# Kernel optimization log

Hardware: AMD Instinct MI355X
Metric: run time of the kernel (lower is better)

## Reference

```python
import jax, jax.numpy as jnp
import numpy as np
from jax import lax

D_MODEL = 1024
D_STATE = 16
D_CONV = 4
EXPAND = 2
D_INNER = EXPAND * D_MODEL  # 2048
DT_RANK = -(-D_MODEL // 16)  # ceil = 64
BATCH = 2
T = 1024


def setup_inputs() -> dict:
    key = jax.random.key(0)
    ks = jax.random.split(key, 9)
    s = 0.02
    x = jax.random.normal(ks[0], (BATCH, T, D_MODEL), dtype=jnp.float32)
    W_in = jax.random.normal(ks[1], (D_MODEL, 2 * D_INNER), dtype=jnp.float32) * s
    conv_w = jax.random.normal(ks[2], (D_INNER, D_CONV), dtype=jnp.float32) * 0.2
    conv_b = jax.random.normal(ks[3], (D_INNER,), dtype=jnp.float32) * 0.02
    W_xproj = jax.random.normal(ks[4], (D_INNER, DT_RANK + 2 * D_STATE), dtype=jnp.float32) * s
    W_dt = jax.random.normal(ks[5], (DT_RANK, D_INNER), dtype=jnp.float32) * s
    b_dt = jax.random.normal(ks[6], (D_INNER,), dtype=jnp.float32) * 0.02
    A_log = jnp.broadcast_to(jnp.log(jnp.arange(1, D_STATE + 1, dtype=jnp.float32)), (D_INNER, D_STATE)).copy()
    D_param = jnp.ones((D_INNER,), dtype=jnp.float32)
    W_out = jax.random.normal(ks[7], (D_INNER, D_MODEL), dtype=jnp.float32) * s
    return {"x": x, "W_in": W_in, "conv_w": conv_w, "conv_b": conv_b,
            "W_xproj": W_xproj, "W_dt": W_dt, "b_dt": b_dt,
            "A_log": A_log, "D_param": D_param, "W_out": W_out}


def _silu(u):
    return u * jax.nn.sigmoid(u)


def _forward(x, W_in, conv_w, conv_b, W_xproj, W_dt, b_dt, A_log, D_param, W_out):
    B, Tlen, _ = x.shape
    # in_proj and split into x-branch and gate z
    xz = x @ W_in                                   # (B,T,2*d_inner)
    x_b, z = jnp.split(xz, 2, axis=-1)              # each (B,T,d_inner)
    # causal depthwise conv1d: y[t] = sum_k w[:,k] * x[t-d_conv+1+k]
    xpad = jnp.pad(x_b, ((0, 0), (D_CONV - 1, 0), (0, 0)))
    xc = conv_b
    for k in range(D_CONV):
        xc = xc + xpad[:, k:k + Tlen, :] * conv_w[:, k]
    xc = _silu(xc)                                  # (B,T,d_inner)
    # SSM parameter projections
    proj = xc @ W_xproj                             # (B,T,dt_rank+2*d_state)
    delta_raw = proj[..., :DT_RANK]
    B_in = proj[..., DT_RANK:DT_RANK + D_STATE]     # (B,T,d_state)
    C_in = proj[..., DT_RANK + D_STATE:]            # (B,T,d_state)
    delta = jax.nn.softplus(delta_raw @ W_dt + b_dt)  # (B,T,d_inner)
    A = -jnp.exp(A_log)                             # (d_inner,d_state)
    A_bar = jnp.exp(delta[..., None] * A)           # (B,T,d_inner,d_state)
    Bx = delta[..., None] * B_in[:, :, None, :] * xc[..., None]  # (B,T,d_inner,d_state)

    def step(h, ins):
        a_t, bx_t, c_t, xc_t = ins
        h = a_t * h + bx_t                          # (B,d_inner,d_state)
        y_t = jnp.einsum('bds,bs->bd', h, c_t) + D_param * xc_t
        return h, y_t

    h0 = jnp.zeros((B, D_INNER, D_STATE), dtype=x.dtype)
    ins = (jnp.swapaxes(A_bar, 0, 1), jnp.swapaxes(Bx, 0, 1),
           jnp.swapaxes(C_in, 0, 1), jnp.swapaxes(xc, 0, 1))
    _, ys = lax.scan(step, h0, ins)                 # ys: (T,B,d_inner)
    y = jnp.swapaxes(ys, 0, 1) * _silu(z)           # gated
    return y @ W_out                                # (B,T,d_model)


def reference(x, W_in, conv_w, conv_b, W_xproj, W_dt, b_dt, A_log, D_param, W_out):
    return _forward(x, W_in, conv_w, conv_b, W_xproj, W_dt, b_dt, A_log, D_param, W_out)
```

## Files before the change

kernel.cpp:

```cpp
#include <hip/hip_runtime.h>
#include <math.h>

#define BATCH   2
#define TLEN    1024
#define DMODEL  1024
#define DINNER  2048
#define DSTATE  16
#define DTRANK  64
#define NPROJ   (DTRANK + 2*DSTATE)
#define CH      16
#define NCH     (TLEN / CH)

typedef __attribute__((ext_vector_type(8))) short short8;
typedef __attribute__((ext_vector_type(4))) float f32x4;

__device__ __forceinline__ float siluf(float u) {
    return u / (1.0f + __expf(-u));
}
__device__ __forceinline__ float softplusf(float x) {
    return (x > 20.0f) ? x : log1pf(__expf(x));
}
__device__ __forceinline__ unsigned short f2bf(float f) {
    union { float f; unsigned u; } v; v.f = f;
    unsigned r = v.u + 0x7FFF + ((v.u >> 16) & 1);
    return (unsigned short)(r >> 16);
}
__device__ __forceinline__ float bf2f(unsigned short u) {
    union { unsigned u; float f; } v; v.u = (unsigned)u << 16;
    return v.f;
}

#define GLOAD_LDS16(g, l) \
  __builtin_amdgcn_global_load_lds( \
     (const __attribute__((address_space(1))) unsigned int*)(g), \
     (__attribute__((address_space(3))) unsigned int*)(l), 16, 0, 0)

template<int NFRAG, int OUTBF>
__global__ __launch_bounds__(256)
void gemm_bf16(const unsigned short* __restrict__ A,
               const unsigned short* __restrict__ BT,
               void* __restrict__ Cv, int ldc, int K)
{
    constexpr int BN = NFRAG * 32;
    __shared__ unsigned short As[128 * 32];
    __shared__ unsigned short Bs[BN * 32];

    const int nwg = gridDim.x * gridDim.y;
    int id = blockIdx.y * gridDim.x + blockIdx.x;
    {
        const int q = nwg >> 3, r = nwg & 7, xcd = id & 7, lid = id >> 3;
        id = (xcd < r ? xcd * (q + 1) : r * (q + 1) + (xcd - r) * q) + lid;
    }
    const int bx = id % gridDim.x, by = id / gridDim.x;

    const int tid  = threadIdx.x;
    const int wid  = tid >> 6;
    const int lane = tid & 63;
    const int brow = by * 128;
    const int bcol = bx * BN;
    const int wr = (wid >> 1) * 64;
    const int wc = (wid & 1) * (NFRAG * 16);
    const int lrow = lane & 15;
    const int lk   = (lane >> 4) * 8;

    f32x4 acc[4][NFRAG] = {};

    for (int k0 = 0; k0 < K; k0 += 32) {
        #pragma unroll
        for (int it = 0; it < 2; ++it) {
            const int c = it * 256 + tid;
            const unsigned short* g = A + (size_t)(brow + (c >> 2)) * K + k0 + (c & 3) * 8;
            GLOAD_LDS16(g, As + (size_t)(it * 256 + wid * 64) * 8);
        }
        #pragma unroll
        for (int it = 0; it < BN / 64; ++it) {
            const int c = it * 256 + tid;
            const unsigned short* g = BT + (size_t)(bcol + (c >> 2)) * K + k0 + (c & 3) * 8;
            GLOAD_LDS16(g, Bs + (size_t)(it * 256 + wid * 64) * 8);
        }
        __syncthreads();

        short8 af[4], bfr[NFRAG];
        #pragma unroll
        for (int m = 0; m < 4; ++m)
            af[m] = *(const short8*)(As + (size_t)(wr + m * 16 + lrow) * 32 + lk);
        #pragma unroll
        for (int n = 0; n < NFRAG; ++n)
            bfr[n] = *(const short8*)(Bs + (size_t)(wc + n * 16 + lrow) * 32 + lk);

        #pragma unroll
        for (int m = 0; m < 4; ++m)
            #pragma unroll
            for (int n = 0; n < NFRAG; ++n)
                acc[m][n] = __builtin_amdgcn_mfma_f32_16x16x32_bf16(af[m], bfr[n], acc[m][n], 0, 0, 0);
        __syncthreads();
    }

    const int crow = (lane >> 4) * 4;
    #pragma unroll
    for (int m = 0; m < 4; ++m)
        #pragma unroll
        for (int n = 0; n < NFRAG; ++n) {
            const size_t coff = (size_t)(brow + wr + m * 16 + crow) * ldc + bcol + wc + n * 16 + lrow;
            #pragma unroll
            for (int r = 0; r < 4; ++r) {
                if (OUTBF)
                    ((unsigned short*)Cv)[coff + (size_t)r * ldc] = f2bf(acc[m][n][r]);
                else
                    ((float*)Cv)[coff + (size_t)r * ldc] = acc[m][n][r];
            }
        }
}

template<int EPI, int ABF, int OUTBF>
__global__ __launch_bounds__(256)
void gemm_f32(const void* __restrict__ Av, int lda,
              const float* __restrict__ B, int ldb,
              void* __restrict__ Cv, int ldc,
              int N, int kchunk,
              const float* __restrict__ bias, size_t zstride)
{
    __shared__ float As[16][64 + 4];
    __shared__ float Bs[16][64 + 4];
    const int tid  = threadIdx.x;
    const int brow = blockIdx.y * 64;
    const int bcol = blockIdx.x * 64;
    const int kbeg = blockIdx.z * kchunk;
    const size_t cofs = (size_t)blockIdx.z * zstride;
    const int tr = ((tid >> 4) & 15) << 2;
    const int tc = (tid & 15) << 2;
    const int ar = tid >> 2;
    const int ac = (tid & 3) << 2;
    const int br = tid >> 4;
    const int bc = (tid & 15) << 2;

    float acc[4][4] = {{0.f,0.f,0.f,0.f},{0.f,0.f,0.f,0.f},
                       {0.f,0.f,0.f,0.f},{0.f,0.f,0.f,0.f}};

    for (int k0 = kbeg; k0 < kbeg + kchunk; k0 += 16) {
        float4 av;
        if (ABF) {
            const unsigned short* Ab = (const unsigned short*)Av;
            ushort4 t = *(const ushort4*)(Ab + (size_t)(brow + ar) * lda + k0 + ac);
            av = make_float4(bf2f(t.x), bf2f(t.y), bf2f(t.z), bf2f(t.w));
        } else {
            av = *(const float4*)((const float*)Av + (size_t)(brow + ar) * lda + k0 + ac);
        }
        As[ac+0][ar] = av.x; As[ac+1][ar] = av.y;
        As[ac+2][ar] = av.z; As[ac+3][ar] = av.w;

        float4 bv = make_float4(0.f, 0.f, 0.f, 0.f);
        if (bcol + bc < N)
            bv = *(const float4*)(B + (size_t)(k0 + br) * ldb + bcol + bc);
        *(float4*)&Bs[br][bc] = bv;

        __syncthreads();
        #pragma unroll
        for (int k = 0; k < 16; ++k) {
            float4 a4 = *(const float4*)&As[k][tr];
            float4 b4 = *(const float4*)&Bs[k][tc];
            float am[4] = {a4.x, a4.y, a4.z, a4.w};
            float bn[4] = {b4.x, b4.y, b4.z, b4.w};
            #pragma unroll
            for (int m = 0; m < 4; ++m)
                #pragma unroll
                for (int n = 0; n < 4; ++n)
                    acc[m][n] = fmaf(am[m], bn[n], acc[m][n]);
        }
        __syncthreads();
    }

    #pragma unroll
    for (int m = 0; m < 4; ++m) {
        const int gr = brow + tr + m;
        #pragma unroll
        for (int n = 0; n < 4; ++n) {
            const int gc = bcol + tc + n;
            if (gc < N) {
                float v = acc[m][n];
                if (EPI == 1) v = softplusf(v + bias[gc]);
                if (OUTBF)
                    ((unsigned short*)Cv)[cofs + (size_t)gr * ldc + gc] = f2bf(v);
                else
                    ((float*)Cv)[cofs + (size_t)gr * ldc + gc] = v;
            }
        }
    }
}

__global__ __launch_bounds__(256)
void reduce8(const float* __restrict__ in, float* __restrict__ out, int n, size_t zstride)
{
    const int i = blockIdx.x * 256 + threadIdx.x;
    if (i >= n) return;
    float s = 0.f;
    #pragma unroll
    for (int z = 0; z < 8; ++z) s += in[(size_t)z * zstride + i];
    out[i] = s;
}

__global__ __launch_bounds__(256)
void cast_rn(const float* __restrict__ in, unsigned short* __restrict__ out)
{
    const int i = blockIdx.x * 256 + threadIdx.x;
    float4 v = ((const float4*)in)[i];
    union { unsigned short u[4]; uint2 v2; } o;
    o.u[0] = f2bf(v.x); o.u[1] = f2bf(v.y); o.u[2] = f2bf(v.z); o.u[3] = f2bf(v.w);
    ((uint2*)out)[i] = o.v2;
}

__global__ __launch_bounds__(256)
void transpose_cast(const float* __restrict__ in, unsigned short* __restrict__ out,
                    int R, int C)
{
    __shared__ float tile[32][33];
    const int tx = threadIdx.x & 31, ty = threadIdx.x >> 5;
    const int c0 = blockIdx.x * 32, r0 = blockIdx.y * 32;
    #pragma unroll
    for (int j = 0; j < 32; j += 8)
        tile[ty + j][tx] = in[(size_t)(r0 + ty + j) * C + c0 + tx];
    __syncthreads();
    #pragma unroll
    for (int j = 0; j < 32; j += 8)
        out[(size_t)(c0 + ty + j) * R + r0 + tx] = f2bf(tile[tx][ty + j]);
}

__global__ __launch_bounds__(256)
void conv_silu(const unsigned short* __restrict__ xz, const float* __restrict__ conv_w,
               const float* __restrict__ conv_b, unsigned short* __restrict__ xc)
{
    const int idx = blockIdx.x * 256 + threadIdx.x;
    const int d = idx & (DINNER - 1);
    const int t = (idx >> 11) & (TLEN - 1);
    const int b = idx >> 21;

    const unsigned short* xb = xz + (size_t)b * TLEN * (2*DINNER) + d;
    float s = conv_b[d];
    const float4 w = *(const float4*)(conv_w + d * 4);
    const float wk[4] = {w.x, w.y, w.z, w.w};
    #pragma unroll
    for (int k = 0; k < 4; ++k) {
        const int tt = t + k - 3;
        if (tt >= 0) s = fmaf(bf2f(xb[(size_t)tt * (2*DINNER)]), wk[k], s);
    }
    xc[idx] = f2bf(siluf(s));
}

__global__ __launch_bounds__(256)
void scan1(const unsigned short* __restrict__ delta, const unsigned short* __restrict__ xc,
           const float* __restrict__ proj, const float* __restrict__ A_log,
           float* __restrict__ hloc, float* __restrict__ sumdel)
{
    const int idx = blockIdx.x * 256 + threadIdx.x;
    const int d = idx & (DINNER - 1);
    const int c = (idx >> 11) & (NCH - 1);
    const int b = idx >> 17;

    float Aa[DSTATE];
    #pragma unroll
    for (int s = 0; s < DSTATE; ++s) Aa[s] = -__expf(A_log[d * DSTATE + s]);

    float h[DSTATE];
    #pragma unroll
    for (int s = 0; s < DSTATE; ++s) h[s] = 0.f;
    float sd = 0.f;

    const int t0 = c * CH;
    const unsigned short* dptr = delta + ((size_t)(b * TLEN + t0)) * DINNER + d;
    const unsigned short* xptr = xc    + ((size_t)(b * TLEN + t0)) * DINNER + d;
    const float* pptr = proj  + ((size_t)(b * TLEN + t0)) * NPROJ;

    for (int t = 0; t < CH; ++t) {
        const float dl = bf2f(dptr[(size_t)t * DINNER]);
        const float xv = bf2f(xptr[(size_t)t * DINNER]);
        const float dx = dl * xv;
        sd += dl;
        #pragma unroll
        for (int s = 0; s < DSTATE; ++s) {
            const float ab = __expf(dl * Aa[s]);
            const float Bv = pptr[t * NPROJ + DTRANK + s];
            h[s] = fmaf(ab, h[s], dx * Bv);
        }
    }
    const size_t base = (((size_t)(b * DINNER + d)) * NCH + c) * DSTATE;
    float4* hp = (float4*)(hloc + base);
    hp[0] = make_float4(h[0],  h[1],  h[2],  h[3]);
    hp[1] = make_float4(h[4],  h[5],  h[6],  h[7]);
    hp[2] = make_float4(h[8],  h[9],  h[10], h[11]);
    hp[3] = make_float4(h[12], h[13], h[14], h[15]);
    sumdel[(size_t)(b * DINNER + d) * NCH + c] = sd;
}

__global__ __launch_bounds__(256)
void scan_combine(const float* __restrict__ hloc, const float* __restrict__ sumdel,
                  const float* __restrict__ A_log, float* __restrict__ hstart)
{
    __shared__ float hl[64 * 17];
    __shared__ float hs[64 * 17];
    const int bd   = blockIdx.x;
    const int d    = bd & (DINNER - 1);
    const int tid  = threadIdx.x;
    const int lane = tid & 63;
    const int w    = tid >> 6;

    const size_t gbase = (size_t)bd * NCH * DSTATE;
    {
        const float4 v = ((const float4*)(hloc + gbase))[tid];
        const int c = tid >> 2, s0 = (tid & 3) * 4;
        hl[c*17 + s0+0] = v.x; hl[c*17 + s0+1] = v.y;
        hl[c*17 + s0+2] = v.z; hl[c*17 + s0+3] = v.w;
    }
    const float sd = sumdel[(size_t)bd * NCH + lane];
    __syncthreads();

    #pragma unroll
    for (int q = 0; q < 4; ++q) {
        const int s = w * 4 + q;
        const float Aa = -__expf(A_log[d * DSTATE + s]);
        float A  = __expf(Aa * sd);
        float Bv = hl[lane*17 + s];
        #pragma unroll
        for (int off = 1; off < 64; off <<= 1) {
            float Ap = __shfl_up(A, off);
            float Bp = __shfl_up(Bv, off);
            if (lane >= off) { Bv = fmaf(A, Bp, Bv); A *= Ap; }
        }
        float hsv = __shfl_up(Bv, 1);
        if (lane == 0) hsv = 0.f;
        hs[lane*17 + s] = hsv;
    }
    __syncthreads();
    {
        const int c = tid >> 2, s0 = (tid & 3) * 4;
        float4 v = make_float4(hs[c*17 + s0+0], hs[c*17 + s0+1],
                               hs[c*17 + s0+2], hs[c*17 + s0+3]);
        ((float4*)(hstart + gbase))[tid] = v;
    }
}

__global__ __launch_bounds__(256)
void scan2(const unsigned short* __restrict__ delta, const unsigned short* __restrict__ xc,
           const float* __restrict__ proj, const float* __restrict__ A_log,
           const float* __restrict__ D_param, const unsigned short* __restrict__ xz,
           const float* __restrict__ hstart, unsigned short* __restrict__ y)
{
    const int idx = blockIdx.x * 256 + threadIdx.x;
    const int d = idx & (DINNER - 1);
    const int c = (idx >> 11) & (NCH - 1);
    const int b = idx >> 17;

    float Aa[DSTATE];
    #pragma unroll
    for (int s = 0; s < DSTATE; ++s) Aa[s] = -__expf(A_log[d * DSTATE + s]);

    float h[DSTATE];
    const size_t hbase = (((size_t)(b * DINNER + d)) * NCH + c) * DSTATE;
    {
        const float4* hp = (const float4*)(hstart + hbase);
        float4 v0 = hp[0], v1 = hp[1], v2 = hp[2], v3 = hp[3];
        h[0]=v0.x; h[1]=v0.y; h[2]=v0.z; h[3]=v0.w;
        h[4]=v1.x; h[5]=v1.y; h[6]=v1.z; h[7]=v1.w;
        h[8]=v2.x; h[9]=v2.y; h[10]=v2.z; h[11]=v2.w;
        h[12]=v3.x; h[13]=v3.y; h[14]=v3.z; h[15]=v3.w;
    }

    const float Dp = D_param[d];
    const int t0 = c * CH;
    const unsigned short* dptr = delta + ((size_t)(b * TLEN + t0)) * DINNER + d;
    const unsigned short* xptr = xc    + ((size_t)(b * TLEN + t0)) * DINNER + d;
    const float* pptr = proj  + ((size_t)(b * TLEN + t0)) * NPROJ;
    const unsigned short* zptr = xz + ((size_t)(b * TLEN + t0)) * (2*DINNER) + DINNER + d;
    unsigned short* yptr = y + ((size_t)(b * TLEN + t0)) * DINNER + d;

    for (int t = 0; t < CH; ++t) {
        const float dl = bf2f(dptr[(size_t)t * DINNER]);
        const float xv = bf2f(xptr[(size_t)t * DINNER]);
        const float dx = dl * xv;
        float yt = 0.f;
        #pragma unroll
        for (int s = 0; s < DSTATE; ++s) {
            const float ab = __expf(dl * Aa[s]);
            const float Bv = pptr[t * NPROJ + DTRANK + s];
            h[s] = fmaf(ab, h[s], dx * Bv);
            const float Cv = pptr[t * NPROJ + DTRANK + DSTATE + s];
            yt = fmaf(h[s], Cv, yt);
        }
        yt = fmaf(Dp, xv, yt);
        const float z = bf2f(zptr[(size_t)t * (2*DINNER)]);
        yptr[(size_t)t * DINNER] = f2bf(yt * siluf(z));
    }
}

extern "C" void kernel_launch(void* const* d_in, const int* in_sizes, int n_in,
                              void* d_out, int out_size, void* d_ws, size_t ws_size,
                              hipStream_t stream)
{
    const float* x      = (const float*)d_in[0];
    const float* W_in   = (const float*)d_in[1];
    const float* conv_w = (const float*)d_in[2];
    const float* conv_b = (const float*)d_in[3];
    const float* W_xproj= (const float*)d_in[4];
    const float* W_dt   = (const float*)d_in[5];
    const float* b_dt   = (const float*)d_in[6];
    const float* A_log  = (const float*)d_in[7];
    const float* D_param= (const float*)d_in[8];
    const float* W_out  = (const float*)d_in[9];
    float* out = (float*)d_out;

    float* ws = (float*)d_ws;
    unsigned short* xz_bf    = (unsigned short*)ws;
    unsigned short* xc_bf    = (unsigned short*)(ws + 4194304);
    float*          proj     = ws + 6291456;
    unsigned short* delta_bf = (unsigned short*)(ws + 6488064);
    float*          hloc     = ws + 8585216;
    float*          sumdel   = ws + 12779520;
    float*          hstart   = ws + 13041664;
    float*          projp    = hloc;
    unsigned short* x_bf     = (unsigned short*)hstart;
    unsigned short* wt_in    = (unsigned short*)(hstart + 1048576);
    unsigned short* yb_bf    = (unsigned short*)hloc;
    unsigned short* wt_out   = (unsigned short*)(hloc + 2097152);

    dim3 blk(256);

    cast_rn<<<(BATCH*TLEN*DMODEL/4)/256, blk, 0, stream>>>(x, x_bf);
    transpose_cast<<<dim3(2*DINNER/32, DMODEL/32), blk, 0, stream>>>(W_in, wt_in, DMODEL, 2*DINNER);
    gemm_bf16<4,1><<<dim3(2*DINNER/128, 2048/128), blk, 0, stream>>>(x_bf, wt_in, xz_bf, 2*DINNER, DMODEL);

    conv_silu<<<(BATCH*TLEN*DINNER)/256, blk, 0, stream>>>(xz_bf, conv_w, conv_b, xc_bf);

    gemm_f32<0,1,0><<<dim3(2, 2048/64, 8), blk, 0, stream>>>(
        xc_bf, DINNER, W_xproj, NPROJ, projp, NPROJ, NPROJ, DINNER/8, nullptr, 196608);
    reduce8<<<(196608 + 255)/256, blk, 0, stream>>>(projp, proj, 196608, 196608);

    gemm_f32<1,0,1><<<dim3(2048/64, 2048/64), blk, 0, stream>>>(
        proj, NPROJ, W_dt, DINNER, delta_bf, DINNER, DINNER, DTRANK, b_dt, 0);

    scan1<<<(BATCH*NCH*DINNER)/256, blk, 0, stream>>>(delta_bf, xc_bf, proj, A_log, hloc, sumdel);
    scan_combine<<<BATCH*DINNER, blk, 0, stream>>>(hloc, sumdel, A_log, hstart);
    transpose_cast<<<dim3(DMODEL/32, DINNER/32), blk, 0, stream>>>(W_out, wt_out, DINNER, DMODEL);
    scan2<<<(BATCH*NCH*DINNER)/256, blk, 0, stream>>>(delta_bf, xc_bf, proj, A_log, D_param, xz_bf, hstart, yb_bf);

    gemm_bf16<2,0><<<dim3(DMODEL/64, 2048/128), blk, 0, stream>>>(yb_bf, wt_out, out, DMODEL, DINNER);
}
```

Measured before the change: 291.1 us.

## Move x_proj and dt_proj GEMMs onto bf16 MFMA kernel with split-K

```diff
diff --git a/kernel.cpp b/kernel.cpp
--- a/kernel.cpp
+++ b/kernel.cpp
@@ -35,11 +35,12 @@
      (const __attribute__((address_space(1))) unsigned int*)(g), \
      (__attribute__((address_space(3))) unsigned int*)(l), 16, 0, 0)
 
-template<int NFRAG, int OUTBF>
-__global__ __launch_bounds__(256)
-void gemm_bf16(const unsigned short* __restrict__ A,
-               const unsigned short* __restrict__ BT,
-               void* __restrict__ Cv, int ldc, int K)
+template<int NFRAG, int OUTBF, int EPI>
+__global__ __launch_bounds__(256)
+void gemm_bf16(const unsigned short* __restrict__ A, int lda,
+               const unsigned short* __restrict__ BT, int ldb,
+               void* __restrict__ Cv, int ldc, int kchunk,
+               const float* __restrict__ bias, size_t zstride)
 {
     constexpr int BN = NFRAG * 32;
     __shared__ unsigned short As[128 * 32];
@@ -58,6 +59,7 @@
     const int lane = tid & 63;
     const int brow = by * 128;
     const int bcol = bx * BN;
+    const int kbeg = blockIdx.z * kchunk;
     const int wr = (wid >> 1) * 64;
     const int wc = (wid & 1) * (NFRAG * 16);
     const int lrow = lane & 15;
@@ -65,18 +67,21 @@
 
     f32x4 acc[4][NFRAG] = {};
 
-    for (int k0 = 0; k0 < K; k0 += 32) {
+    for (int k0 = kbeg; k0 < kbeg + kchunk; k0 += 32) {
         #pragma unroll
         for (int it = 0; it < 2; ++it) {
             const int c = it * 256 + tid;
-            const unsigned short* g = A + (size_t)(brow + (c >> 2)) * K + k0 + (c & 3) * 8;
+            const unsigned short* g = A + (size_t)(brow + (c >> 2)) * lda + k0 + (c & 3) * 8;
             GLOAD_LDS16(g, As + (size_t)(it * 256 + wid * 64) * 8);
         }
-        #pragma unroll
-        for (int it = 0; it < BN / 64; ++it) {
+        constexpr int BCH = BN * 4;
+        #pragma unroll
+        for (int it = 0; it < (BCH + 255) / 256; ++it) {
             const int c = it * 256 + tid;
-            const unsigned short* g = BT + (size_t)(bcol + (c >> 2)) * K + k0 + (c & 3) * 8;
-            GLOAD_LDS16(g, Bs + (size_t)(it * 256 + wid * 64) * 8);
+            if (BCH % 256 == 0 || c < BCH) {
+                const unsigned short* g = BT + (size_t)(bcol + (c >> 2)) * ldb + k0 + (c & 3) * 8;
+                GLOAD_LDS16(g, Bs + (size_t)(it * 256 + wid * 64) * 8);
+            }
         }
         __syncthreads();
 
@@ -96,100 +101,29 @@
         __syncthreads();
     }
 
+    const size_t zoff = (size_t)blockIdx.z * zstride;
     const int crow = (lane >> 4) * 4;
     #pragma unroll
     for (int m = 0; m < 4; ++m)
         #pragma unroll
         for (int n = 0; n < NFRAG; ++n) {
-            const size_t coff = (size_t)(brow + wr + m * 16 + crow) * ldc + bcol + wc + n * 16 + lrow;
+            const int gc = bcol + wc + n * 16 + lrow;
+            const size_t coff = zoff + (size_t)(brow + wr + m * 16 + crow) * ldc + gc;
             #pragma unroll
             for (int r = 0; r < 4; ++r) {
-                if (OUTBF)
-                    ((unsigned short*)Cv)[coff + (size_t)r * ldc] = f2bf(acc[m][n][r]);
-                else
-                    ((float*)Cv)[coff + (size_t)r * ldc] = acc[m][n][r];
-            }
-        }
-}
-
-template<int EPI, int ABF, int OUTBF>
-__global__ __launch_bounds__(256)
-void gemm_f32(const void* __restrict__ Av, int lda,
-              const float* __restrict__ B, int ldb,
-              void* __restrict__ Cv, int ldc,
-              int N, int kchunk,
-              const float* __restrict__ bias, size_t zstride)
-{
-    __shared__ float As[16][64 + 4];
-    __shared__ float Bs[16][64 + 4];
-    const int tid  = threadIdx.x;
-    const int brow = blockIdx.y * 64;
-    const int bcol = blockIdx.x * 64;
-    const int kbeg = blockIdx.z * kchunk;
-    const size_t cofs = (size_t)blockIdx.z * zstride;
-    const int tr = ((tid >> 4) & 15) << 2;
-    const int tc = (tid & 15) << 2;
-    const int ar = tid >> 2;
-    const int ac = (tid & 3) << 2;
-    const int br = tid >> 4;
-    const int bc = (tid & 15) << 2;
-
-    float acc[4][4] = {{0.f,0.f,0.f,0.f},{0.f,0.f,0.f,0.f},
-                       {0.f,0.f,0.f,0.f},{0.f,0.f,0.f,0.f}};
-
-    for (int k0 = kbeg; k0 < kbeg + kchunk; k0 += 16) {
-        float4 av;
-        if (ABF) {
-            const unsigned short* Ab = (const unsigned short*)Av;
-            ushort4 t = *(const ushort4*)(Ab + (size_t)(brow + ar) * lda + k0 + ac);
-            av = make_float4(bf2f(t.x), bf2f(t.y), bf2f(t.z), bf2f(t.w));
-        } else {
-            av = *(const float4*)((const float*)Av + (size_t)(brow + ar) * lda + k0 + ac);
-        }
-        As[ac+0][ar] = av.x; As[ac+1][ar] = av.y;
-        As[ac+2][ar] = av.z; As[ac+3][ar] = av.w;
-
-        float4 bv = make_float4(0.f, 0.f, 0.f, 0.f);
-        if (bcol + bc < N)
-            bv = *(const float4*)(B + (size_t)(k0 + br) * ldb + bcol + bc);
-        *(float4*)&Bs[br][bc] = bv;
-
-        __syncthreads();
-        #pragma unroll
-        for (int k = 0; k < 16; ++k) {
-            float4 a4 = *(const float4*)&As[k][tr];
-            float4 b4 = *(const float4*)&Bs[k][tc];
-            float am[4] = {a4.x, a4.y, a4.z, a4.w};
-            float bn[4] = {b4.x, b4.y, b4.z, b4.w};
-            #pragma unroll
-            for (int m = 0; m < 4; ++m)
-                #pragma unroll
-                for (int n = 0; n < 4; ++n)
-                    acc[m][n] = fmaf(am[m], bn[n], acc[m][n]);
-        }
-        __syncthreads();
-    }
-
-    #pragma unroll
-    for (int m = 0; m < 4; ++m) {
-        const int gr = brow + tr + m;
-        #pragma unroll
-        for (int n = 0; n < 4; ++n) {
-            const int gc = bcol + tc + n;
-            if (gc < N) {
-                float v = acc[m][n];
+                float v = acc[m][n][r];
                 if (EPI == 1) v = softplusf(v + bias[gc]);
                 if (OUTBF)
-                    ((unsigned short*)Cv)[cofs + (size_t)gr * ldc + gc] = f2bf(v);
+                    ((unsigned short*)Cv)[coff + (size_t)r * ldc] = f2bf(v);
                 else
-                    ((float*)Cv)[cofs + (size_t)gr * ldc + gc] = v;
+                    ((float*)Cv)[coff + (size_t)r * ldc] = v;
             }
         }
-    }
-}
-
-__global__ __launch_bounds__(256)
-void reduce8(const float* __restrict__ in, float* __restrict__ out, int n, size_t zstride)
+}
+
+__global__ __launch_bounds__(256)
+void reduce8_dual(const float* __restrict__ in, float* __restrict__ out,
+                  unsigned short* __restrict__ draw, int n, size_t zstride)
 {
     const int i = blockIdx.x * 256 + threadIdx.x;
     if (i >= n) return;
@@ -197,6 +131,9 @@
     #pragma unroll
     for (int z = 0; z < 8; ++z) s += in[(size_t)z * zstride + i];
     out[i] = s;
+    const int row = i / NPROJ;
+    const int col = i - row * NPROJ;
+    if (col < DTRANK) draw[(size_t)row * DTRANK + col] = f2bf(s);
 }
 
 __global__ __launch_bounds__(256)
@@ -416,30 +353,37 @@
     float*          sumdel   = ws + 12779520;
     float*          hstart   = ws + 13041664;
     float*          projp    = hloc;
+    unsigned short* draw_bf  = (unsigned short*)(hloc + 1572864);
+    unsigned short* yb_bf    = (unsigned short*)hloc;
+    unsigned short* wt_out   = (unsigned short*)(hloc + 2097152);
     unsigned short* x_bf     = (unsigned short*)hstart;
     unsigned short* wt_in    = (unsigned short*)(hstart + 1048576);
-    unsigned short* yb_bf    = (unsigned short*)hloc;
-    unsigned short* wt_out   = (unsigned short*)(hloc + 2097152);
+    unsigned short* wxp_t    = (unsigned short*)(hstart + 3145728);
+    unsigned short* wdt_t    = (unsigned short*)(hstart + 3244032);
 
     dim3 blk(256);
 
-    cast_rn<<<(BATCH*TLEN*DMODEL/4)/256, blk, 0, stream>>>(x, x_bf);
+    cast_rn<<<2048, blk, 0, stream>>>(x, x_bf);
     transpose_cast<<<dim3(2*DINNER/32, DMODEL/32), blk, 0, stream>>>(W_in, wt_in, DMODEL, 2*DINNER);
-    gemm_bf16<4,1><<<dim3(2*DINNER/128, 2048/128), blk, 0, stream>>>(x_bf, wt_in, xz_bf, 2*DINNER, DMODEL);
+    gemm_bf16<4,1,0><<<dim3(2*DINNER/128, 2048/128), blk, 0, stream>>>(
+        x_bf, DMODEL, wt_in, DMODEL, xz_bf, 2*DINNER, DMODEL, nullptr, 0);
 
     conv_silu<<<(BATCH*TLEN*DINNER)/256, blk, 0, stream>>>(xz_bf, conv_w, conv_b, xc_bf);
 
-    gemm_f32<0,1,0><<<dim3(2, 2048/64, 8), blk, 0, stream>>>(
-        xc_bf, DINNER, W_xproj, NPROJ, projp, NPROJ, NPROJ, DINNER/8, nullptr, 196608);
-    reduce8<<<(196608 + 255)/256, blk, 0, stream>>>(projp, proj, 196608, 196608);
-
-    gemm_f32<1,0,1><<<dim3(2048/64, 2048/64), blk, 0, stream>>>(
-        proj, NPROJ, W_dt, DINNER, delta_bf, DINNER, DINNER, DTRANK, b_dt, 0);
+    transpose_cast<<<dim3(NPROJ/32, DINNER/32), blk, 0, stream>>>(W_xproj, wxp_t, DINNER, NPROJ);
+    gemm_bf16<3,0,0><<<dim3(1, 2048/128, 8), blk, 0, stream>>>(
+        xc_bf, DINNER, wxp_t, DINNER, projp, NPROJ, DINNER/8, nullptr, 196608);
+    reduce8_dual<<<768, blk, 0, stream>>>(projp, proj, draw_bf, 196608, 196608);
+
+    transpose_cast<<<dim3(DINNER/32, DTRANK/32), blk, 0, stream>>>(W_dt, wdt_t, DTRANK, DINNER);
+    gemm_bf16<4,1,1><<<dim3(2048/128, 2048/128), blk, 0, stream>>>(
+        draw_bf, DTRANK, wdt_t, DTRANK, delta_bf, DINNER, DTRANK, b_dt, 0);
 
     scan1<<<(BATCH*NCH*DINNER)/256, blk, 0, stream>>>(delta_bf, xc_bf, proj, A_log, hloc, sumdel);
     scan_combine<<<BATCH*DINNER, blk, 0, stream>>>(hloc, sumdel, A_log, hstart);
     transpose_cast<<<dim3(DMODEL/32, DINNER/32), blk, 0, stream>>>(W_out, wt_out, DINNER, DMODEL);
     scan2<<<(BATCH*NCH*DINNER)/256, blk, 0, stream>>>(delta_bf, xc_bf, proj, A_log, D_param, xz_bf, hstart, yb_bf);
 
-    gemm_bf16<2,0><<<dim3(DMODEL/64, 2048/128), blk, 0, stream>>>(yb_bf, wt_out, out, DMODEL, DINNER);
-}
+    gemm_bf16<2,0,0><<<dim3(DMODEL/64, 2048/128), blk, 0, stream>>>(
+        yb_bf, DINNER, wt_out, DINNER, out, DMODEL, DINNER, nullptr, 0);
+}
```

Result: faster. 284.6 us (-2.2%).
